# Optimization experiments

Hardware: AMD Instinct MI355X
Metric: run time of the kernel (lower is better)

Reference implementation:

```python
import jax, jax.numpy as jnp
import numpy as np

B, D, H, W = 4, 40, 40, 40
NPB = 12000            # active voxels per batch item
C0, C1 = 32, 64        # nPlanes = [32, 64]
BLOCK_REPS = 2
EPS = 1e-4             # BatchNorm eps used by the gorilla-3d norm_fn


def _subm_pairs(coords, dims):
    # indice pairs for 3x3x3 submanifold conv: for kernel offset k,
    # out[j] += f[i] @ W[k] where coord_j = coord_i + offset_k and both voxels are active
    D_, H_, W_ = dims
    b, z, y, x = coords[:, 0], coords[:, 1], coords[:, 2], coords[:, 3]
    lin = ((b * D_ + z) * H_ + y) * W_ + x  # sorted unique linear ids
    ins, outs = [], []
    for dz in (-1, 0, 1):
        for dy in (-1, 0, 1):
            for dx in (-1, 0, 1):
                nz, ny, nx = z + dz, y + dy, x + dx
                valid = (nz >= 0) & (nz < D_) & (ny >= 0) & (ny < H_) & (nx >= 0) & (nx < W_)
                tgt = ((b * D_ + nz) * H_ + ny) * W_ + nx
                pos = np.clip(np.searchsorted(lin, tgt), 0, len(lin) - 1)
                found = valid & (lin[pos] == tgt)
                ins.append(np.nonzero(found)[0].astype(np.int32))
                outs.append(pos[found].astype(np.int32))
    return ins, outs


def _down_pairs(coords, dims):
    # indice pairs for 2x2x2 stride-2 SparseConv3d; output voxels = unique(coord // 2)
    D_, H_, W_ = dims
    D2, H2, W2 = (D_ + 1) // 2, (H_ + 1) // 2, (W_ + 1) // 2
    b, z, y, x = coords[:, 0], coords[:, 1], coords[:, 2], coords[:, 3]
    plin = ((b * D2 + z // 2) * H2 + y // 2) * W2 + x // 2
    ulin, inv = np.unique(plin, return_inverse=True)
    k = (z % 2) * 4 + (y % 2) * 2 + (x % 2)  # which of the 8 kernel taps
    ins = [np.nonzero(k == kk)[0].astype(np.int32) for kk in range(8)]
    outs = [inv[m].astype(np.int32) for m in ins]
    t = ulin.copy()
    x1 = t % W2; t //= W2; y1 = t % H2; t //= H2; z1 = t % D2; b1 = t // D2
    coords1 = np.stack([b1, z1, y1, x1], 1).astype(np.int64)
    return ins, outs, coords1, (D2, H2, W2)


def _pad_pairs(ins, outs, pad_in, pad_out):
    K = len(ins); P = max(max(len(p) for p in ins), 1)
    A = np.full((K, P), pad_in, np.int32)
    O = np.full((K, P), pad_out, np.int32)
    for kk in range(K):
        A[kk, :len(ins[kk])] = ins[kk]
        O[kk, :len(outs[kk])] = outs[kk]
    return jnp.asarray(A), jnp.asarray(O)


def setup_inputs():
    rng = np.random.default_rng(0)
    coords = []
    for b in range(B):
        lin = np.sort(rng.choice(D * H * W, NPB, replace=False))
        z = lin // (H * W); y = (lin // W) % H; x = lin % W
        coords.append(np.stack([np.full(NPB, b), z, y, x], 1))
    coords = np.concatenate(coords).astype(np.int64)
    n0 = coords.shape[0]
    s0i, s0o = _subm_pairs(coords, (D, H, W))
    subm0_in, subm0_out = _pad_pairs(s0i, s0o, n0, n0)
    di, do, coords1, dims1 = _down_pairs(coords, (D, H, W))
    n1 = int(coords1.shape[0])
    down_in, down_out = _pad_pairs(di, do, n0, n1)
    s1i, s1o = _subm_pairs(coords1, dims1)
    subm1_in, subm1_out = _pad_pairs(s1i, s1o, n1, n1)

    keys = iter(jax.random.split(jax.random.key(0), 128))

    def bn_p(c):
        g = 1.0 + 0.1 * jax.random.normal(next(keys), (c,))
        be = 0.1 * jax.random.normal(next(keys), (c,))
        m = 0.1 * jax.random.normal(next(keys), (c,))
        v = jax.random.uniform(next(keys), (c,), minval=0.5, maxval=1.5)
        return jnp.stack([g, be, m, v]).astype(jnp.float32)

    def w(shape):
        fan = shape[-2] * (shape[-3] if len(shape) >= 3 else 1)
        return (jax.random.normal(next(keys), shape) / np.sqrt(fan)).astype(jnp.float32)

    return dict(
        feats=jax.random.normal(next(keys), (n0, C0), dtype=jnp.float32),
        res0_W=w((BLOCK_REPS, 2, 27, C0, C0)),
        res0_bn=jnp.stack([jnp.stack([bn_p(C0), bn_p(C0)]) for _ in range(BLOCK_REPS)]),
        down_bn=bn_p(C0), down_W=w((8, C0, C1)),
        res1_W=w((BLOCK_REPS, 2, 27, C1, C1)),
        res1_bn=jnp.stack([jnp.stack([bn_p(C1), bn_p(C1)]) for _ in range(BLOCK_REPS)]),
        up_bn=bn_p(C1), up_W=w((8, C1, C0)),
        tail0_bn1=bn_p(2 * C0), tail0_W1=w((27, 2 * C0, C0)),
        tail0_bn2=bn_p(C0), tail0_W2=w((27, C0, C0)),
        tail0_Wsc=w((2 * C0, C0)),
        tail1_W=w((2, 27, C0, C0)),
        tail1_bn=jnp.stack([bn_p(C0), bn_p(C0)]),
        subm0_in=subm0_in, subm0_out=subm0_out,
        subm1_in=subm1_in, subm1_out=subm1_out,
        down_in=down_in, down_out=down_out,
        n1=n1,
    )


def _bn_relu(x, p):
    # BatchNorm1d (eval mode, running stats) followed by ReLU; p is [4, C] = (gamma, beta, mean, var)
    g, b, m, v = p
    return jax.nn.relu((x - m) * (g * jax.lax.rsqrt(v + EPS)) + b)


def _sparse_conv(x, Wk, pin, pout, n_out):
    # gather-matmul-scatter over padded indice pairs.
    # x: [Nin, Cin], Wk: [K, Cin, Cout], pin/pout: [K, P] (padded with sentinel Nin / n_out)
    x_ext = jnp.concatenate([x, jnp.zeros((1, x.shape[1]), x.dtype)], 0)
    g = x_ext[pin]                                   # [K, P, Cin]
    c = jnp.einsum('kpc,kcd->kpd', g, Wk)            # [K, P, Cout]
    out = jnp.zeros((n_out + 1, Wk.shape[2]), x.dtype)
    out = out.at[pout.reshape(-1)].add(c.reshape(-1, Wk.shape[2]))
    return out[:n_out]


def _res_block(x, Ws, bns, pin, pout, n, Wsc=None):
    # ResidualBlock: (norm, relu, subm3x3, norm, relu, subm3x3) + identity/1x1 shortcut
    idt = x if Wsc is None else x @ Wsc
    h = _bn_relu(x, bns[0]); h = _sparse_conv(h, Ws[0], pin, pout, n)
    h = _bn_relu(h, bns[1]); h = _sparse_conv(h, Ws[1], pin, pout, n)
    return h + idt


def _forward(feats, res0_W, res0_bn, down_bn, down_W, res1_W, res1_bn, up_bn, up_W,
             tail0_bn1, tail0_W1, tail0_bn2, tail0_W2, tail0_Wsc, tail1_W, tail1_bn,
             subm0_in, subm0_out, subm1_in, subm1_out, down_in, down_out, n1):
    n0 = feats.shape[0]
    x = feats
    for i in range(BLOCK_REPS):                       # self.blocks
        x = _res_block(x, res0_W[i], res0_bn[i], subm0_in, subm0_out, n0)
    identity = x                                      # identity SparseConvTensor
    # self.conv: norm, relu, SparseConv3d(k=2, s=2)
    x1 = _sparse_conv(_bn_relu(x, down_bn), down_W, down_in, down_out, n1)
    for i in range(BLOCK_REPS):                       # self.u (leaf UBlock) blocks
        x1 = _res_block(x1, res1_W[i], res1_bn[i], subm1_in, subm1_out, n1)
    # self.deconv: norm, relu, SparseInverseConv3d (same pairs, roles swapped)
    dec = _sparse_conv(_bn_relu(x1, up_bn), up_W, down_out, down_in, n0)
    x = jnp.concatenate([identity, dec], 1)           # [N0, 2*C0]
    # blocks_tail: block0 (2*C0 -> C0, 1x1 shortcut), block1 (C0 -> C0)
    h = _bn_relu(x, tail0_bn1); h = _sparse_conv(h, tail0_W1, subm0_in, subm0_out, n0)
    h = _bn_relu(h, tail0_bn2); h = _sparse_conv(h, tail0_W2, subm0_in, subm0_out, n0)
    x = h + x @ tail0_Wsc
    x = _res_block(x, tail1_W, tail1_bn, subm0_in, subm0_out, n0)
    return x


def reference(feats, res0_W, res0_bn, down_bn, down_W, res1_W, res1_bn, up_bn, up_W,
              tail0_bn1, tail0_W1, tail0_bn2, tail0_W2, tail0_Wsc, tail1_W, tail1_bn,
              subm0_in, subm0_out, subm1_in, subm1_out, down_in, down_out, n1):
    return _forward(feats, res0_W, res0_bn, down_bn, down_W, res1_W, res1_bn, up_bn, up_W,
                    tail0_bn1, tail0_W1, tail0_bn2, tail0_W2, tail0_Wsc, tail1_W, tail1_bn,
                    subm0_in, subm0_out, subm1_in, subm1_out, down_in, down_out, n1)
```

## Files before the change

### kernel.cpp

```cpp
#include <hip/hip_runtime.h>

#define EPS_BN 1e-4f

typedef _Float16 f16x8 __attribute__((ext_vector_type(8)));
typedef float f32x4 __attribute__((ext_vector_type(4)));

template <int C>
__global__ __launch_bounds__(256) void bn_relu_kernel(
    const float* __restrict__ x, const float* __restrict__ bn,
    _Float16* __restrict__ out, int n_const, const int* __restrict__ n_dev)
{
    const int n = n_dev ? *n_dev : n_const;
    const long total = (long)n * C;
    const long i = (long)blockIdx.x * blockDim.x + threadIdx.x;
    if (i >= total) return;
    const int c = (int)(i & (C - 1));
    const float g = bn[c], b = bn[C + c], m = bn[2 * C + c], v = bn[3 * C + c];
    const float val = (x[i] - m) * (g * rsqrtf(v + EPS_BN)) + b;
    out[i] = (_Float16)fmaxf(val, 0.f);
}

__global__ __launch_bounds__(256) void build_table_kernel(
    const int* __restrict__ pin, const int* __restrict__ pout,
    int K, int P, int pad_const, const int* __restrict__ pad_dev,
    int KPAD, int* __restrict__ T)
{
    const int e = blockIdx.x * 256 + threadIdx.x;
    if (e >= K * P) return;
    const int pad = pad_dev ? *pad_dev : pad_const;
    const int in = pin[e];
    if (in == pad) return;
    const int k = e / P;
    T[(size_t)pout[e] * KPAD + k] = in;
}

__global__ __launch_bounds__(256) void wcvt_kernel(
    const float* __restrict__ src, _Float16* __restrict__ dst,
    int K, int CIN, int COUT)
{
    const int e = blockIdx.x * 256 + threadIdx.x;
    if (e >= K * CIN * COUT) return;
    const int k = e / (CIN * COUT), r = e % (CIN * COUT);
    const int ci = r / COUT, co = r % COUT;
    dst[(size_t)k * CIN * COUT + (size_t)co * CIN + ci] = (_Float16)src[e];
}

template <int CIN, int COUT, int K, int KPAD, int WR, int WC, int M_REP>
__global__ __launch_bounds__(512, 4) void mconv_kernel(
    const _Float16* __restrict__ x, const _Float16* __restrict__ Wt,
    const int* __restrict__ Trow,
    const float* __restrict__ add, float* __restrict__ fout,
    const float* __restrict__ bnx, _Float16* __restrict__ hout,
    int n_const, const int* __restrict__ n_dev)
{
    constexpr int BM = WR * M_REP * 16;
    constexpr int KK = CIN / 32;
    constexpr int SLOTS = BM * CIN / 8;
    constexpr int SPT = (SLOTS + 511) / 512;
    constexpr int SEGS = CIN / 8;
    __shared__ _Float16 A[2][SLOTS * 8];
    __shared__ int TL[BM * K];

    const int n = n_dev ? *n_dev : n_const;
    const int row0 = blockIdx.x * BM;
    if (row0 >= n) return;

    const int tid = threadIdx.x;
    const int wave = tid >> 6, lane = tid & 63;
    const int lrow = lane & 15, g = lane >> 4;
    const int wr = wave / WC, wc = wave % WC;

    for (int idx = tid; idx < BM * K; idx += 512) {
        const int r = idx / K, k = idx % K;
        TL[idx] = (row0 + r < n) ? Trow[(size_t)(row0 + r) * KPAD + k] : -1;
    }
    __syncthreads();

    auto stage_issue = [&](int k, f16x8 (&v)[SPT]) {
#pragma unroll
        for (int s = 0; s < SPT; ++s) {
            const int slot = tid + s * 512;
            if (slot < SLOTS) {
                const int r = slot / SEGS, seg = slot % SEGS;
                const int t = TL[r * K + k];
                v[s] = (t >= 0) ? *(const f16x8*)(x + (size_t)t * CIN + seg * 8)
                                : (f16x8)(_Float16)0.f;
            }
        }
    };
    auto stage_write = [&](int buf, f16x8 (&v)[SPT]) {
#pragma unroll
        for (int s = 0; s < SPT; ++s) {
            const int slot = tid + s * 512;
            if (slot < SLOTS) {
                const int r = slot / SEGS, seg = slot % SEGS;
                const int a16 = ((r >> 4) * KK + (seg >> 2)) * 64 +
                                (seg & 3) * 16 + (r & 15);
                const int sw = a16 ^ ((a16 >> 4) & 7);
                *(f16x8*)(&A[buf][sw * 8]) = v[s];
            }
        }
    };

    f32x4 acc[M_REP];
#pragma unroll
    for (int m = 0; m < M_REP; ++m) acc[m] = (f32x4)0.f;

    f16x8 st[SPT];
    stage_issue(0, st);
    stage_write(0, st);
    __syncthreads();

    for (int k = 0; k < K; ++k) {
        f16x8 nst[SPT];
        if (k + 1 < K) stage_issue(k + 1, nst);

        const _Float16* wb = Wt + ((size_t)k * COUT + wc * 16 + lrow) * CIN + g * 8;
        f16x8 b[KK];
#pragma unroll
        for (int kk = 0; kk < KK; ++kk) b[kk] = *(const f16x8*)(wb + kk * 32);

        const _Float16* Ab = A[k & 1];
#pragma unroll
        for (int m = 0; m < M_REP; ++m) {
#pragma unroll
            for (int kk = 0; kk < KK; ++kk) {
                const int a16 = ((wr * M_REP + m) * KK + kk) * 64 + lane;
                const int sw = a16 ^ ((a16 >> 4) & 7);
                const f16x8 av = *(const f16x8*)(&Ab[sw * 8]);
                acc[m] = __builtin_amdgcn_mfma_f32_16x16x32_f16(av, b[kk], acc[m],
                                                                0, 0, 0);
            }
        }

        if (k + 1 < K) stage_write((k + 1) & 1, nst);
        __syncthreads();
    }

#pragma unroll
    for (int m = 0; m < M_REP; ++m) {
        const int rbase = row0 + (wr * M_REP + m) * 16 + g * 4;
        const int c = wc * 16 + lrow;
        float sc = 0.f, mm = 0.f, be = 0.f;
        if (hout) {
            const float ga = bnx[c], va = bnx[3 * COUT + c];
            be = bnx[COUT + c];
            mm = bnx[2 * COUT + c];
            sc = ga * rsqrtf(va + EPS_BN);
        }
#pragma unroll
        for (int i = 0; i < 4; ++i) {
            const int r = rbase + i;
            if (r < n) {
                const size_t o = (size_t)r * COUT + c;
                float v = acc[m][i];
                if (add) v += add[o];
                if (fout) fout[o] = v;
                if (hout) hout[o] = (_Float16)fmaxf((v - mm) * sc + be, 0.f);
            }
        }
    }
}

__global__ __launch_bounds__(256) void concat_bn_kernel(
    const float* __restrict__ a, const float* __restrict__ b,
    float* __restrict__ fout, const float* __restrict__ bnx,
    _Float16* __restrict__ hout, int n)
{
    const int i = blockIdx.x * 256 + threadIdx.x;
    if (i >= n * 64) return;
    const int row = i >> 6, c = i & 63;
    const float v = (c < 32) ? a[row * 32 + c] : b[row * 32 + (c - 32)];
    fout[i] = v;
    const float g = bnx[c], be = bnx[64 + c], m = bnx[128 + c], va = bnx[192 + c];
    hout[i] = (_Float16)fmaxf((v - m) * (g * rsqrtf(va + EPS_BN)) + be, 0.f);
}

__global__ __launch_bounds__(256) void dense_mm_kernel(
    const float* __restrict__ x, const float* __restrict__ W,
    float* __restrict__ out, int n)
{
    __shared__ float Wl[64 * 32];
    for (int i = threadIdx.x; i < 64 * 32; i += 256) Wl[i] = W[i];
    __syncthreads();
    const int idx = blockIdx.x * 256 + threadIdx.x;
    const int row = idx >> 5, c = idx & 31;
    if (row >= n) return;
    const float* xr = x + (size_t)row * 64;
    float acc = 0.f;
#pragma unroll
    for (int q = 0; q < 16; ++q) {
        const float4 xv = *(const float4*)(xr + 4 * q);
        acc = fmaf(xv.x, Wl[(4 * q + 0) * 32 + c], acc);
        acc = fmaf(xv.y, Wl[(4 * q + 1) * 32 + c], acc);
        acc = fmaf(xv.z, Wl[(4 * q + 2) * 32 + c], acc);
        acc = fmaf(xv.w, Wl[(4 * q + 3) * 32 + c], acc);
    }
    out[(size_t)row * 32 + c] = acc;
}


extern "C" void kernel_launch(void* const* d_in, const int* in_sizes, int n_in,
                              void* d_out, int out_size, void* d_ws, size_t ws_size,
                              hipStream_t stream)
{
    const float* feats   = (const float*)d_in[0];
    const float* res0_W  = (const float*)d_in[1];
    const float* res0_bn = (const float*)d_in[2];
    const float* down_bn = (const float*)d_in[3];
    const float* down_W  = (const float*)d_in[4];
    const float* res1_W  = (const float*)d_in[5];
    const float* res1_bn = (const float*)d_in[6];
    const float* up_bn   = (const float*)d_in[7];
    const float* up_W    = (const float*)d_in[8];
    const float* t0_bn1  = (const float*)d_in[9];
    const float* t0_W1   = (const float*)d_in[10];
    const float* t0_bn2  = (const float*)d_in[11];
    const float* t0_W2   = (const float*)d_in[12];
    const float* t0_Wsc  = (const float*)d_in[13];
    const float* t1_W    = (const float*)d_in[14];
    const float* t1_bn   = (const float*)d_in[15];
    const int* s0i = (const int*)d_in[16];
    const int* s0o = (const int*)d_in[17];
    const int* s1i = (const int*)d_in[18];
    const int* s1o = (const int*)d_in[19];
    const int* dni = (const int*)d_in[20];
    const int* dno = (const int*)d_in[21];
    const int* n1p = (const int*)d_in[22];

    const int n0 = in_sizes[0] / 32;
    const int P0 = in_sizes[16] / 27;
    const int P1 = in_sizes[18] / 27;
    const int Pd = in_sizes[20] / 8;

    const size_t bufN = (size_t)n0 * 64;
    float* F1 = (float*)d_ws;
    float* F2 = F1 + bufN;
    float* F3 = F2 + bufN;
    float* F4 = F3 + bufN;
    _Float16* Ha = (_Float16*)(F4 + bufN);
    _Float16* Hb = Ha + bufN;
    int* T0r = (int*)(Hb + bufN);
    int* T1r = T0r + (size_t)n0 * 28;
    int* Tdr = T1r + (size_t)n0 * 28;
    int* Tur = Tdr + (size_t)n0 * 8;
    _Float16* Wt_res0 = (_Float16*)(Tur + (size_t)n0 * 8);
    _Float16* Wt_down = Wt_res0 + 108 * 1024;
    _Float16* Wt_res1 = Wt_down + 8 * 2048;
    _Float16* Wt_up   = Wt_res1 + (size_t)108 * 4096;
    _Float16* Wt_t01  = Wt_up + 8 * 2048;
    _Float16* Wt_t02  = Wt_t01 + 27 * 2048;
    _Float16* Wt_t1   = Wt_t02 + 27 * 1024;

    hipMemsetAsync(T0r, 0xFF, (size_t)n0 * 28 * 4, stream);
    hipMemsetAsync(T1r, 0xFF, (size_t)n0 * 28 * 4, stream);
    hipMemsetAsync(Tdr, 0xFF, (size_t)n0 * 8 * 4, stream);
    hipMemsetAsync(Tur, 0xFF, (size_t)n0 * 8 * 4, stream);
    auto build = [&](const int* pin, const int* pout, int K, int P,
                     int padc, const int* padd, int KPAD, int* T) {
        hipLaunchKernelGGL(build_table_kernel, dim3((K * P + 255) / 256),
                           dim3(256), 0, stream, pin, pout, K, P, padc, padd,
                           KPAD, T);
    };
    build(s0i, s0o, 27, P0, n0, nullptr, 28, T0r);
    build(s1i, s1o, 27, P1, 0, n1p, 28, T1r);
    build(dni, dno, 8, Pd, n0, nullptr, 8, Tdr);
    build(dno, dni, 8, Pd, 0, n1p, 8, Tur);

    auto wcvt = [&](const float* src, _Float16* dst, int K, int CI, int CO) {
        const int tot = K * CI * CO;
        hipLaunchKernelGGL(wcvt_kernel, dim3((tot + 255) / 256), dim3(256), 0,
                           stream, src, dst, K, CI, CO);
    };
    wcvt(res0_W, Wt_res0, 108, 32, 32);
    wcvt(down_W, Wt_down, 8, 32, 64);
    wcvt(res1_W, Wt_res1, 108, 64, 64);
    wcvt(up_W,   Wt_up,   8, 64, 32);
    wcvt(t0_W1,  Wt_t01, 27, 64, 32);
    wcvt(t0_W2,  Wt_t02, 27, 32, 32);
    wcvt(t1_W,   Wt_t1,  54, 32, 32);

    const int g32 = (n0 * 32 + 255) / 256;
    const int g64 = (n0 * 64 + 255) / 256;
    const int gm128 = (n0 + 127) / 128;
    const int gm64  = (n0 + 63) / 64;

    auto mc3232 = [&](const _Float16* xin, const _Float16* Wtp, const int* T,
                      const float* add, float* fo, const float* bn, _Float16* ho,
                      int nc, const int* nd) {
        hipLaunchKernelGGL((mconv_kernel<32, 32, 27, 28, 4, 2, 2>), dim3(gm128),
                           dim3(512), 0, stream, xin, Wtp, T, add, fo, bn, ho,
                           nc, nd);
    };
    auto mc6464 = [&](const _Float16* xin, const _Float16* Wtp,
                      const float* add, float* fo, const float* bn, _Float16* ho) {
        hipLaunchKernelGGL((mconv_kernel<64, 64, 27, 28, 2, 4, 2>), dim3(gm64),
                           dim3(512), 0, stream, xin, Wtp, T1r, add, fo, bn, ho,
                           0, n1p);
    };

    hipLaunchKernelGGL((bn_relu_kernel<32>), dim3(g32), dim3(256), 0, stream,
                       feats, res0_bn + 0 * 128, Ha, n0, nullptr);
    mc3232(Ha, Wt_res0 + 0 * 27 * 1024, T0r, nullptr, nullptr,
           res0_bn + 1 * 128, Hb, n0, nullptr);
    mc3232(Hb, Wt_res0 + 1 * 27 * 1024, T0r, feats, F2,
           res0_bn + 2 * 128, Ha, n0, nullptr);
    mc3232(Ha, Wt_res0 + 2 * 27 * 1024, T0r, nullptr, nullptr,
           res0_bn + 3 * 128, Hb, n0, nullptr);
    mc3232(Hb, Wt_res0 + 3 * 27 * 1024, T0r, F2, F3, down_bn, Ha, n0, nullptr);
    hipLaunchKernelGGL((mconv_kernel<32, 64, 8, 8, 2, 4, 2>), dim3(gm64),
                       dim3(512), 0, stream, Ha, Wt_down, Tdr,
                       (const float*)nullptr, F1, res1_bn + 0 * 256, Hb, 0, n1p);
    mc6464(Hb, Wt_res1 + 0 * 27 * 4096, nullptr, nullptr, res1_bn + 1 * 256, Ha);
    mc6464(Ha, Wt_res1 + 1 * 27 * 4096, F1, F4, res1_bn + 2 * 256, Hb);
    mc6464(Hb, Wt_res1 + 2 * 27 * 4096, nullptr, nullptr, res1_bn + 3 * 256, Ha);
    mc6464(Ha, Wt_res1 + 3 * 27 * 4096, F4, F1, up_bn, Hb);
    hipLaunchKernelGGL((mconv_kernel<64, 32, 8, 8, 4, 2, 2>), dim3(gm128),
                       dim3(512), 0, stream, Hb, Wt_up, Tur,
                       (const float*)nullptr, F2, (const float*)nullptr,
                       (_Float16*)nullptr, n0, nullptr);
    hipLaunchKernelGGL(concat_bn_kernel, dim3(g64), dim3(256), 0, stream,
                       F3, F2, F4, t0_bn1, Ha, n0);
    hipLaunchKernelGGL((mconv_kernel<64, 32, 27, 28, 4, 2, 2>), dim3(gm128),
                       dim3(512), 0, stream, Ha, Wt_t01, T0r,
                       (const float*)nullptr, (float*)nullptr, t0_bn2, Hb,
                       n0, nullptr);
    hipLaunchKernelGGL(dense_mm_kernel, dim3(g32), dim3(256), 0, stream,
                       F4, t0_Wsc, F2, n0);
    mc3232(Hb, Wt_t02, T0r, F2, F2, t1_bn + 0 * 128, Ha, n0, nullptr);
    mc3232(Ha, Wt_t1 + 0 * 27 * 1024, T0r, nullptr, nullptr,
           t1_bn + 1 * 128, Hb, n0, nullptr);
    mc3232(Hb, Wt_t1 + 1 * 27 * 1024, T0r, F2, (float*)d_out,
           nullptr, nullptr, n0, nullptr);
}
```

Before: 528.6 us.

## Stage multiple kernel taps per pipeline step with smaller 256-thread blocks

The sparse conv kernel now gathers TG kernel taps into shared memory per pipeline step instead of one. This cuts the number of __syncthreads barriers and lets more gather loads be in flight at once. Blocks shrink to 4 waves with smaller row tiles, so more blocks launch. The LDS XOR swizzle is dropped and s_setprio is raised around the MFMA section. The four table memsets and seven weight-conversion launches are each merged into one launch. In exchange, each block uses more registers and LDS, and removing the swizzle may add LDS bank conflicts.

```diff
diff --git a/kernel.cpp b/kernel.cpp
--- a/kernel.cpp
+++ b/kernel.cpp
@@ -34,31 +34,38 @@
     T[(size_t)pout[e] * KPAD + k] = in;
 }
 
-__global__ __launch_bounds__(256) void wcvt_kernel(
-    const float* __restrict__ src, _Float16* __restrict__ dst,
-    int K, int CIN, int COUT)
-{
-    const int e = blockIdx.x * 256 + threadIdx.x;
-    if (e >= K * CIN * COUT) return;
-    const int k = e / (CIN * COUT), r = e % (CIN * COUT);
-    const int ci = r / COUT, co = r % COUT;
-    dst[(size_t)k * CIN * COUT + (size_t)co * CIN + ci] = (_Float16)src[e];
-}
-
-template <int CIN, int COUT, int K, int KPAD, int WR, int WC, int M_REP>
-__global__ __launch_bounds__(512, 4) void mconv_kernel(
+struct WSeg { const float* src; _Float16* dst; int tot, ci, co; };
+struct WAll { WSeg s[7]; };
+
+__global__ __launch_bounds__(256) void wcvt_all_kernel(WAll w)
+{
+    const WSeg sg = w.s[blockIdx.y];
+    const int per = sg.ci * sg.co;
+    for (int e = blockIdx.x * 256 + threadIdx.x; e < sg.tot; e += gridDim.x * 256) {
+        const int k = e / per, r = e % per;
+        const int ci = r / sg.co, co = r % sg.co;
+        sg.dst[(size_t)k * per + (size_t)co * sg.ci + ci] = (_Float16)sg.src[e];
+    }
+}
+
+template <int CIN, int COUT, int K, int KPAD, int WR, int WC, int M_REP,
+          int TG, int MINW>
+__global__ __launch_bounds__(256, MINW) void mconv_kernel(
     const _Float16* __restrict__ x, const _Float16* __restrict__ Wt,
     const int* __restrict__ Trow,
     const float* __restrict__ add, float* __restrict__ fout,
     const float* __restrict__ bnx, _Float16* __restrict__ hout,
     int n_const, const int* __restrict__ n_dev)
 {
+    static_assert(K % TG == 0, "K must be divisible by TG");
+    static_assert(WR * WC == 4, "4 waves");
     constexpr int BM = WR * M_REP * 16;
     constexpr int KK = CIN / 32;
-    constexpr int SLOTS = BM * CIN / 8;
-    constexpr int SPT = (SLOTS + 511) / 512;
     constexpr int SEGS = CIN / 8;
-    __shared__ _Float16 A[2][SLOTS * 8];
+    constexpr int SLOTS = BM * SEGS;
+    constexpr int SPT = (SLOTS + 255) / 256;
+    constexpr int NP = K / TG;
+    __shared__ _Float16 A[2][TG * SLOTS * 8];
     __shared__ int TL[BM * K];
 
     const int n = n_dev ? *n_dev : n_const;
@@ -70,70 +77,82 @@
     const int lrow = lane & 15, g = lane >> 4;
     const int wr = wave / WC, wc = wave % WC;
 
-    for (int idx = tid; idx < BM * K; idx += 512) {
+    for (int idx = tid; idx < BM * K; idx += 256) {
         const int r = idx / K, k = idx % K;
         TL[idx] = (row0 + r < n) ? Trow[(size_t)(row0 + r) * KPAD + k] : -1;
     }
     __syncthreads();
 
-    auto stage_issue = [&](int k, f16x8 (&v)[SPT]) {
-#pragma unroll
-        for (int s = 0; s < SPT; ++s) {
-            const int slot = tid + s * 512;
-            if (slot < SLOTS) {
-                const int r = slot / SEGS, seg = slot % SEGS;
-                const int t = TL[r * K + k];
-                v[s] = (t >= 0) ? *(const f16x8*)(x + (size_t)t * CIN + seg * 8)
-                                : (f16x8)(_Float16)0.f;
+    auto stage_issue = [&](int p, f16x8 (&v)[TG][SPT]) {
+#pragma unroll
+        for (int tg = 0; tg < TG; ++tg)
+#pragma unroll
+            for (int s = 0; s < SPT; ++s) {
+                const int slot = tid + s * 256;
+                if (slot < SLOTS) {
+                    const int r = slot / SEGS, seg = slot % SEGS;
+                    const int t = TL[r * K + (p * TG + tg)];
+                    v[tg][s] = (t >= 0)
+                        ? *(const f16x8*)(x + (size_t)t * CIN + seg * 8)
+                        : (f16x8)(_Float16)0.f;
+                }
             }
+    };
+    auto stage_write = [&](int buf, f16x8 (&v)[TG][SPT]) {
+#pragma unroll
+        for (int tg = 0; tg < TG; ++tg)
+#pragma unroll
+            for (int s = 0; s < SPT; ++s) {
+                const int slot = tid + s * 256;
+                if (slot < SLOTS) {
+                    const int r = slot / SEGS, seg = slot % SEGS;
+                    const int a16 = tg * SLOTS + ((r >> 4) * KK + (seg >> 2)) * 64
+                                  + (seg & 3) * 16 + (r & 15);
+                    *(f16x8*)(&A[buf][a16 * 8]) = v[tg][s];
+                }
+            }
+    };
+
+    f32x4 acc[M_REP];
+#pragma unroll
+    for (int m = 0; m < M_REP; ++m) acc[m] = (f32x4)0.f;
+
+    {
+        f16x8 st[TG][SPT];
+        stage_issue(0, st);
+        stage_write(0, st);
+    }
+    __syncthreads();
+
+    for (int p = 0; p < NP; ++p) {
+        f16x8 nst[TG][SPT];
+        if (p + 1 < NP) stage_issue(p + 1, nst);
+
+        const _Float16* Ab = A[p & 1];
+        __builtin_amdgcn_s_setprio(1);
+#pragma unroll
+        for (int tg = 0; tg < TG; ++tg) {
+            const int tap = p * TG + tg;
+            const _Float16* wb = Wt + ((size_t)tap * COUT + wc * 16 + lrow) * CIN
+                               + g * 8;
+            f16x8 b[KK];
+#pragma unroll
+            for (int kk = 0; kk < KK; ++kk)
+                b[kk] = *(const f16x8*)(wb + kk * 32);
+#pragma unroll
+            for (int m = 0; m < M_REP; ++m)
+#pragma unroll
+                for (int kk = 0; kk < KK; ++kk) {
+                    const int a16 = tg * SLOTS + ((wr * M_REP + m) * KK + kk) * 64
+                                  + lane;
+                    const f16x8 av = *(const f16x8*)(&Ab[a16 * 8]);
+                    acc[m] = __builtin_amdgcn_mfma_f32_16x16x32_f16(
+                        av, b[kk], acc[m], 0, 0, 0);
+                }
         }
-    };
-    auto stage_write = [&](int buf, f16x8 (&v)[SPT]) {
-#pragma unroll
-        for (int s = 0; s < SPT; ++s) {
-            const int slot = tid + s * 512;
-            if (slot < SLOTS) {
-                const int r = slot / SEGS, seg = slot % SEGS;
-                const int a16 = ((r >> 4) * KK + (seg >> 2)) * 64 +
-                                (seg & 3) * 16 + (r & 15);
-                const int sw = a16 ^ ((a16 >> 4) & 7);
-                *(f16x8*)(&A[buf][sw * 8]) = v[s];
-            }
-        }
-    };
-
-    f32x4 acc[M_REP];
-#pragma unroll
-    for (int m = 0; m < M_REP; ++m) acc[m] = (f32x4)0.f;
-
-    f16x8 st[SPT];
-    stage_issue(0, st);
-    stage_write(0, st);
-    __syncthreads();
-
-    for (int k = 0; k < K; ++k) {
-        f16x8 nst[SPT];
-        if (k + 1 < K) stage_issue(k + 1, nst);
-
-        const _Float16* wb = Wt + ((size_t)k * COUT + wc * 16 + lrow) * CIN + g * 8;
-        f16x8 b[KK];
-#pragma unroll
-        for (int kk = 0; kk < KK; ++kk) b[kk] = *(const f16x8*)(wb + kk * 32);
-
-        const _Float16* Ab = A[k & 1];
-#pragma unroll
-        for (int m = 0; m < M_REP; ++m) {
-#pragma unroll
-            for (int kk = 0; kk < KK; ++kk) {
-                const int a16 = ((wr * M_REP + m) * KK + kk) * 64 + lane;
-                const int sw = a16 ^ ((a16 >> 4) & 7);
-                const f16x8 av = *(const f16x8*)(&Ab[sw * 8]);
-                acc[m] = __builtin_amdgcn_mfma_f32_16x16x32_f16(av, b[kk], acc[m],
-                                                                0, 0, 0);
-            }
-        }
-
-        if (k + 1 < K) stage_write((k + 1) & 1, nst);
+        __builtin_amdgcn_s_setprio(0);
+
+        if (p + 1 < NP) stage_write((p + 1) & 1, nst);
         __syncthreads();
     }
 
@@ -252,10 +271,7 @@
     _Float16* Wt_t02  = Wt_t01 + 27 * 2048;
     _Float16* Wt_t1   = Wt_t02 + 27 * 1024;
 
-    hipMemsetAsync(T0r, 0xFF, (size_t)n0 * 28 * 4, stream);
-    hipMemsetAsync(T1r, 0xFF, (size_t)n0 * 28 * 4, stream);
-    hipMemsetAsync(Tdr, 0xFF, (size_t)n0 * 8 * 4, stream);
-    hipMemsetAsync(Tur, 0xFF, (size_t)n0 * 8 * 4, stream);
+    hipMemsetAsync(T0r, 0xFF, (size_t)n0 * 72 * 4, stream);
     auto build = [&](const int* pin, const int* pout, int K, int P,
                      int padc, const int* padd, int KPAD, int* T) {
         hipLaunchKernelGGL(build_table_kernel, dim3((K * P + 255) / 256),
@@ -267,36 +283,34 @@
     build(dni, dno, 8, Pd, n0, nullptr, 8, Tdr);
     build(dno, dni, 8, Pd, 0, n1p, 8, Tur);
 
-    auto wcvt = [&](const float* src, _Float16* dst, int K, int CI, int CO) {
-        const int tot = K * CI * CO;
-        hipLaunchKernelGGL(wcvt_kernel, dim3((tot + 255) / 256), dim3(256), 0,
-                           stream, src, dst, K, CI, CO);
-    };
-    wcvt(res0_W, Wt_res0, 108, 32, 32);
-    wcvt(down_W, Wt_down, 8, 32, 64);
-    wcvt(res1_W, Wt_res1, 108, 64, 64);
-    wcvt(up_W,   Wt_up,   8, 64, 32);
-    wcvt(t0_W1,  Wt_t01, 27, 64, 32);
-    wcvt(t0_W2,  Wt_t02, 27, 32, 32);
-    wcvt(t1_W,   Wt_t1,  54, 32, 32);
+    WAll wa;
+    wa.s[0] = {res0_W, Wt_res0, 108 * 1024, 32, 32};
+    wa.s[1] = {down_W, Wt_down, 8 * 2048, 32, 64};
+    wa.s[2] = {res1_W, Wt_res1, 108 * 4096, 64, 64};
+    wa.s[3] = {up_W,   Wt_up,   8 * 2048, 64, 32};
+    wa.s[4] = {t0_W1,  Wt_t01,  27 * 2048, 64, 32};
+    wa.s[5] = {t0_W2,  Wt_t02,  27 * 1024, 32, 32};
+    wa.s[6] = {t1_W,   Wt_t1,   54 * 1024, 32, 32};
+    hipLaunchKernelGGL(wcvt_all_kernel, dim3((108 * 4096 + 255) / 256, 7),
+                       dim3(256), 0, stream, wa);
 
     const int g32 = (n0 * 32 + 255) / 256;
     const int g64 = (n0 * 64 + 255) / 256;
-    const int gm128 = (n0 + 127) / 128;
-    const int gm64  = (n0 + 63) / 64;
+    const int gm64 = (n0 + 63) / 64;
+    const int gm32 = (n0 + 31) / 32;
 
     auto mc3232 = [&](const _Float16* xin, const _Float16* Wtp, const int* T,
                       const float* add, float* fo, const float* bn, _Float16* ho,
                       int nc, const int* nd) {
-        hipLaunchKernelGGL((mconv_kernel<32, 32, 27, 28, 4, 2, 2>), dim3(gm128),
-                           dim3(512), 0, stream, xin, Wtp, T, add, fo, bn, ho,
-                           nc, nd);
+        hipLaunchKernelGGL((mconv_kernel<32, 32, 27, 28, 2, 2, 2, 3, 4>),
+                           dim3(gm64), dim3(256), 0, stream,
+                           xin, Wtp, T, add, fo, bn, ho, nc, nd);
     };
     auto mc6464 = [&](const _Float16* xin, const _Float16* Wtp,
                       const float* add, float* fo, const float* bn, _Float16* ho) {
-        hipLaunchKernelGGL((mconv_kernel<64, 64, 27, 28, 2, 4, 2>), dim3(gm64),
-                           dim3(512), 0, stream, xin, Wtp, T1r, add, fo, bn, ho,
-                           0, n1p);
+        hipLaunchKernelGGL((mconv_kernel<64, 64, 27, 28, 1, 4, 2, 3, 4>),
+                           dim3(gm32), dim3(256), 0, stream,
+                           xin, Wtp, T1r, add, fo, bn, ho, 0, n1p);
     };
 
     hipLaunchKernelGGL((bn_relu_kernel<32>), dim3(g32), dim3(256), 0, stream,
@@ -308,21 +322,21 @@
     mc3232(Ha, Wt_res0 + 2 * 27 * 1024, T0r, nullptr, nullptr,
            res0_bn + 3 * 128, Hb, n0, nullptr);
     mc3232(Hb, Wt_res0 + 3 * 27 * 1024, T0r, F2, F3, down_bn, Ha, n0, nullptr);
-    hipLaunchKernelGGL((mconv_kernel<32, 64, 8, 8, 2, 4, 2>), dim3(gm64),
-                       dim3(512), 0, stream, Ha, Wt_down, Tdr,
+    hipLaunchKernelGGL((mconv_kernel<32, 64, 8, 8, 1, 4, 2, 2, 4>),
+                       dim3(gm32), dim3(256), 0, stream, Ha, Wt_down, Tdr,
                        (const float*)nullptr, F1, res1_bn + 0 * 256, Hb, 0, n1p);
     mc6464(Hb, Wt_res1 + 0 * 27 * 4096, nullptr, nullptr, res1_bn + 1 * 256, Ha);
     mc6464(Ha, Wt_res1 + 1 * 27 * 4096, F1, F4, res1_bn + 2 * 256, Hb);
     mc6464(Hb, Wt_res1 + 2 * 27 * 4096, nullptr, nullptr, res1_bn + 3 * 256, Ha);
     mc6464(Ha, Wt_res1 + 3 * 27 * 4096, F4, F1, up_bn, Hb);
-    hipLaunchKernelGGL((mconv_kernel<64, 32, 8, 8, 4, 2, 2>), dim3(gm128),
-                       dim3(512), 0, stream, Hb, Wt_up, Tur,
+    hipLaunchKernelGGL((mconv_kernel<64, 32, 8, 8, 2, 2, 2, 2, 4>),
+                       dim3(gm64), dim3(256), 0, stream, Hb, Wt_up, Tur,
                        (const float*)nullptr, F2, (const float*)nullptr,
                        (_Float16*)nullptr, n0, nullptr);
     hipLaunchKernelGGL(concat_bn_kernel, dim3(g64), dim3(256), 0, stream,
                        F3, F2, F4, t0_bn1, Ha, n0);
-    hipLaunchKernelGGL((mconv_kernel<64, 32, 27, 28, 4, 2, 2>), dim3(gm128),
-                       dim3(512), 0, stream, Ha, Wt_t01, T0r,
+    hipLaunchKernelGGL((mconv_kernel<64, 32, 27, 28, 2, 2, 2, 3, 2>),
+                       dim3(gm64), dim3(256), 0, stream, Ha, Wt_t01, T0r,
                        (const float*)nullptr, (float*)nullptr, t0_bn2, Hb,
                        n0, nullptr);
     hipLaunchKernelGGL(dense_mm_kernel, dim3(g32), dim3(256), 0, stream,
```

Result: no change. 537.9 us (+1.7%).
